# Performance work log

Hardware: AMD Instinct MI355X
Metric: run time of the kernel (lower is better)

The kernel has to match this reference:

```python
import jax, jax.numpy as jnp
import numpy as np
import math

B, T, D_MODEL, N_HEADS = 4, 2048, 1024, 16
HEAD_DIM = D_MODEL // N_HEADS


def setup_inputs() -> dict:
    key = jax.random.key(0)
    k1, k2, k3 = jax.random.split(key, 3)
    x = jax.random.normal(k1, (B, T, D_MODEL), dtype=jnp.float32)
    # torch Linear weight layout: [out_features, in_features]
    w_qkv = jax.random.normal(k2, (3 * D_MODEL, D_MODEL), dtype=jnp.float32) * (1.0 / math.sqrt(D_MODEL))
    w_out = jax.random.normal(k3, (D_MODEL, D_MODEL), dtype=jnp.float32) * (1.0 / math.sqrt(D_MODEL))
    return {"x": x, "w_qkv": w_qkv, "w_out": w_out}


def reference(x, w_qkv, w_out):
    b, t, c = x.shape
    h, d = N_HEADS, HEAD_DIM
    # qkv projection: (B,T,3C) -> (3,B,H,T,D)
    qkv = jnp.einsum('btc,fc->btf', x, w_qkv)
    qkv = qkv.reshape(b, t, 3, h, d).transpose(2, 0, 3, 1, 4)
    q, k, v = qkv[0], qkv[1], qkv[2]
    scale = 1.0 / math.sqrt(d)
    # full O(T^2) attention scores, causal masked
    scores = jnp.einsum('bhqd,bhkd->bhqk', q, k) * scale
    causal = jnp.tril(jnp.ones((t, t), dtype=bool))
    scores = jnp.where(causal[None, None, :, :], scores, jnp.float32(-jnp.inf))
    attn = jax.nn.softmax(scores, axis=-1)
    out = jnp.einsum('bhqk,bhkd->bhqd', attn, v)  # (B,H,T,D)
    out = out.transpose(0, 2, 1, 3).reshape(b, t, c)
    out = jnp.einsum('btc,oc->bto', out, w_out)
    return out
```

## Files before the change

kernel.cpp:

```cpp
#include <hip/hip_runtime.h>
#include <hip/hip_bf16.h>

#define T_SEQ 2048
#define BATCH 4
#define NH    16
#define DM    1024
#define HD    64

typedef __attribute__((ext_vector_type(4))) float  f32x4;
typedef __attribute__((ext_vector_type(8))) short  s16x8;
typedef __attribute__((ext_vector_type(4))) short  s16x4;
typedef __attribute__((ext_vector_type(4))) unsigned short u16x4;

__device__ __forceinline__ unsigned short f2b(float f) {
  union { float f; unsigned u; } v; v.f = f;
  unsigned u = v.u;
  unsigned r = 0x7fffu + ((u >> 16) & 1u);
  u += r;
  return (unsigned short)(u >> 16);
}

__device__ __forceinline__ f32x4 mfma16(s16x8 a, s16x8 b, f32x4 c) {
  return __builtin_amdgcn_mfma_f32_16x16x32_bf16(a, b, c, 0, 0, 0);
}

__global__ void cvt_f32_bf16(const float* __restrict__ src,
                             unsigned short* __restrict__ dst, int n4) {
  int i = blockIdx.x * blockDim.x + threadIdx.x;
  int stride = gridDim.x * blockDim.x;
  for (int j = i; j < n4; j += stride) {
    f32x4 v = ((const f32x4*)src)[j];
    s16x4 o;
    o.x = (short)f2b(v.x); o.y = (short)f2b(v.y);
    o.z = (short)f2b(v.z); o.w = (short)f2b(v.w);
    ((s16x4*)dst)[j] = o;
  }
}

template<int OUT_F32>
__global__ __launch_bounds__(256)
void gemm_bt(const unsigned short* __restrict__ A,
             const unsigned short* __restrict__ B,
             void* __restrict__ C, int M, int N, int K) {
  __shared__ unsigned short As[128 * 32];
  __shared__ unsigned short Bs[128 * 32];
  const int tid  = threadIdx.x;
  const int lane = tid & 63;
  const int w    = tid >> 6;
  const int wr   = w >> 1, wc = w & 1;
  const int lr   = lane & 15, g = lane >> 4;

  const int gx  = gridDim.x, nwg = gx * gridDim.y;
  const int bid = blockIdx.y * gx + blockIdx.x;
  const int qq  = nwg >> 3;
  const int b2  = (bid & 7) * qq + (bid >> 3);
  const int row0 = (b2 % gx) * 128;
  const int col0 = (b2 / gx) * 128;

  const int srow = w * 16 + (lane >> 2);
  const int scol = (lane & 3) * 8;

  f32x4 acc[4][4] = {};

  for (int kt = 0; kt < K; kt += 32) {
    __syncthreads();
#pragma unroll
    for (int s = 0; s < 2; ++s) {
      const unsigned short* srcA = A + (size_t)(row0 + s * 64 + srow) * K + kt + scol;
      __builtin_amdgcn_global_load_lds((const void*)srcA, (void*)&As[(s * 64 + w * 16) * 32], 16, 0, 0);
      const unsigned short* srcB = B + (size_t)(col0 + s * 64 + srow) * K + kt + scol;
      __builtin_amdgcn_global_load_lds((const void*)srcB, (void*)&Bs[(s * 64 + w * 16) * 32], 16, 0, 0);
    }
    __syncthreads();

    s16x8 af[4], bf[4];
#pragma unroll
    for (int m = 0; m < 4; ++m)
      af[m] = *(const s16x8*)&As[(wr * 64 + m * 16 + lr) * 32 + g * 8];
#pragma unroll
    for (int n = 0; n < 4; ++n)
      bf[n] = *(const s16x8*)&Bs[(wc * 64 + n * 16 + lr) * 32 + g * 8];
#pragma unroll
    for (int m = 0; m < 4; ++m)
#pragma unroll
      for (int n = 0; n < 4; ++n)
        acc[m][n] = mfma16(af[m], bf[n], acc[m][n]);
  }

#pragma unroll
  for (int m = 0; m < 4; ++m)
#pragma unroll
    for (int n = 0; n < 4; ++n)
#pragma unroll
      for (int i = 0; i < 4; ++i) {
        int row = row0 + wr * 64 + m * 16 + g * 4 + i;
        int col = col0 + wc * 64 + n * 16 + lr;
        if (OUT_F32)
          ((float*)C)[(size_t)row * N + col] = acc[m][n][i];
        else
          ((unsigned short*)C)[(size_t)row * N + col] = f2b(acc[m][n][i]);
      }
}

__global__ __launch_bounds__(512)
void attn_kernel(const unsigned short* __restrict__ qkv,
                 unsigned short* __restrict__ out) {
  __shared__ unsigned short Ks[2][64 * 64];
  __shared__ unsigned short Vt[2][64 * 72];
  __shared__ unsigned short Ps[8][16 * 72];

  const int tid  = threadIdx.x;
  const int lane = tid & 63;
  const int w    = tid >> 6;
  const int lr   = lane & 15, g = lane >> 4;
  const int bh   = blockIdx.x;
  const int qt   = 15 - (int)blockIdx.y;
  const int b    = bh >> 4, h = bh & 15;
  const int q0   = qt * 128;
  const int qr   = q0 + w * 16;
  const int qq   = qr + lr;
  const size_t rb = (size_t)b * T_SEQ;

  s16x8 qf[2];
  {
    const unsigned short* qp = qkv + (rb + qq) * 3072 + h * 64;
    qf[0] = *(const s16x8*)(qp + g * 8);
    qf[1] = *(const s16x8*)(qp + 32 + g * 8);
  }

  float mI = -1e30f, lI = 0.f;
  f32x4 o[4] = {};

  const int nt   = 2 * qt + 2;
  const int qmax = qr + 15;

  const bool grpV = (tid < 256);
  const int vd0 = (tid & 7) * 8, vr0 = (tid >> 3) * 2;
  const int t2  = tid - 256;
  const int kr0 = t2 >> 3, kc0 = t2 & 7;

  s16x8 pre0, pre1;
  {
    if (grpV) {
      const unsigned short* vp = &qkv[(rb + vr0) * 3072 + 2048 + h * 64 + vd0];
      pre0 = *(const s16x8*)vp;
      pre1 = *(const s16x8*)(vp + 3072);
    } else {
      const unsigned short* kp = &qkv[(rb + kr0) * 3072 + 1024 + h * 64 + kc0 * 8];
      pre0 = *(const s16x8*)kp;
      pre1 = *(const s16x8*)(kp + 32 * 3072);
    }
  }

  for (int t = 0; t < nt; ++t) {
    const int cur = t & 1;
    if (grpV) {
#pragma unroll
      for (int jj = 0; jj < 8; ++jj) {
        int d = vd0 + jj;
        int sw = ((d ^ (d >> 3)) & 7) << 4;
        unsigned val = (unsigned)(unsigned short)pre0[jj] |
                       ((unsigned)(unsigned short)pre1[jj] << 16);
        *(unsigned*)((char*)&Vt[cur][0] + d * 144 + ((vr0 * 2) ^ sw)) = val;
      }
    } else {
      *(s16x8*)((char*)&Ks[cur][0] + kr0 * 128 + ((kc0 * 16) ^ ((kr0 & 7) << 4))) = pre0;
      int kr1 = kr0 + 32;
      *(s16x8*)((char*)&Ks[cur][0] + kr1 * 128 + ((kc0 * 16) ^ ((kr1 & 7) << 4))) = pre1;
    }
    if (t + 1 < nt) {
      const int kv0n = (t + 1) * 64;
      if (grpV) {
        const unsigned short* vp = &qkv[(rb + kv0n + vr0) * 3072 + 2048 + h * 64 + vd0];
        pre0 = *(const s16x8*)vp;
        pre1 = *(const s16x8*)(vp + 3072);
      } else {
        const unsigned short* kp = &qkv[(rb + kv0n + kr0) * 3072 + 1024 + h * 64 + kc0 * 8];
        pre0 = *(const s16x8*)kp;
        pre1 = *(const s16x8*)(kp + 32 * 3072);
      }
    }
    __syncthreads();

    const int kv0 = t * 64;
    if (kv0 <= qmax) {
      f32x4 s4[4];
      __builtin_amdgcn_s_setprio(1);
#pragma unroll
      for (int kc = 0; kc < 4; ++kc) {
        int row = kc * 16 + lr;
        const char* kbase = (const char*)&Ks[cur][0] + row * 128;
        int sw = (row & 7) << 4;
        s16x8 kf0 = *(const s16x8*)(kbase + ((g * 16) ^ sw));
        s16x8 kf1 = *(const s16x8*)(kbase + ((64 + g * 16) ^ sw));
        f32x4 s = {};
        s = mfma16(kf0, qf[0], s);
        s = mfma16(kf1, qf[1], s);
        s4[kc] = s;
      }
      __builtin_amdgcn_s_setprio(0);

#pragma unroll
      for (int kc = 0; kc < 4; ++kc)
#pragma unroll
        for (int i = 0; i < 4; ++i) {
          int key = kv0 + kc * 16 + g * 4 + i;
          float v = s4[kc][i] * 0.125f;
          s4[kc][i] = (key <= qq) ? v : -1e30f;
        }

      float mx0 = fmaxf(fmaxf(s4[0][0], s4[0][1]), fmaxf(s4[0][2], s4[0][3]));
      float mx1 = fmaxf(fmaxf(s4[1][0], s4[1][1]), fmaxf(s4[1][2], s4[1][3]));
      float mx2 = fmaxf(fmaxf(s4[2][0], s4[2][1]), fmaxf(s4[2][2], s4[2][3]));
      float mx3 = fmaxf(fmaxf(s4[3][0], s4[3][1]), fmaxf(s4[3][2], s4[3][3]));
      float mx = fmaxf(fmaxf(mx0, mx1), fmaxf(mx2, mx3));
      mx = fmaxf(mx, __shfl_xor(mx, 16));
      mx = fmaxf(mx, __shfl_xor(mx, 32));
      float mn = fmaxf(mI, mx);
      float alpha = __expf(mI - mn);
      mI = mn;
      float rs = 0.f;
#pragma unroll
      for (int kc = 0; kc < 4; ++kc)
#pragma unroll
        for (int i = 0; i < 4; ++i) {
          float p = __expf(s4[kc][i] - mn);
          s4[kc][i] = p;
          rs += p;
        }
      rs += __shfl_xor(rs, 16);
      rs += __shfl_xor(rs, 32);
      lI = lI * alpha + rs;

      {
        char* pw = (char*)&Ps[w][0] + lr * 144;
#pragma unroll
        for (int kc = 0; kc < 4; ++kc) {
          unsigned v0 = (unsigned)f2b(s4[kc][0]) | ((unsigned)f2b(s4[kc][1]) << 16);
          unsigned v1 = (unsigned)f2b(s4[kc][2]) | ((unsigned)f2b(s4[kc][3]) << 16);
          *(unsigned*)(pw + kc * 32 + g * 8)     = v0;
          *(unsigned*)(pw + kc * 32 + g * 8 + 4) = v1;
        }
      }

#pragma unroll
      for (int n = 0; n < 4; ++n)
#pragma unroll
        for (int i = 0; i < 4; ++i)
          o[n][i] *= alpha;

      asm volatile("s_waitcnt lgkmcnt(0)" ::: "memory");

      __builtin_amdgcn_s_setprio(1);
#pragma unroll
      for (int kk = 0; kk < 2; ++kk) {
        s16x8 pf = *(const s16x8*)((const char*)&Ps[w][0] + lr * 144 + kk * 64 + g * 16);
#pragma unroll
        for (int n = 0; n < 4; ++n) {
          int d = n * 16 + lr;
          int sw = ((d ^ (d >> 3)) & 7) << 4;
          s16x8 vf = *(const s16x8*)((const char*)&Vt[cur][0] + d * 144 + ((kk * 64 + g * 16) ^ sw));
          o[n] = mfma16(vf, pf, o[n]);
        }
      }
      __builtin_amdgcn_s_setprio(0);
    }
  }

  float rl = 1.f / lI;
#pragma unroll
  for (int n = 0; n < 4; ++n) {
    u16x4 pk;
#pragma unroll
    for (int i = 0; i < 4; ++i) pk[i] = f2b(o[n][i] * rl);
    *(u16x4*)&out[(rb + qq) * 1024 + h * 64 + n * 16 + g * 4] = pk;
  }
}

extern "C" void kernel_launch(void* const* d_in, const int* in_sizes, int n_in,
                              void* d_out, int out_size, void* d_ws, size_t ws_size,
                              hipStream_t stream) {
  const float* x     = (const float*)d_in[0];
  const float* w_qkv = (const float*)d_in[1];
  const float* w_out = (const float*)d_in[2];

  const size_t n_x   = (size_t)BATCH * T_SEQ * DM;
  const size_t n_wq  = (size_t)3 * DM * DM;
  const size_t n_wo  = (size_t)DM * DM;
  const size_t n_qkv = (size_t)BATCH * T_SEQ * 3 * DM;
  const size_t need  = (n_x + n_wq + n_wo + n_qkv + n_x) * 2;
  if (ws_size < need) return;

  unsigned short* xb  = (unsigned short*)d_ws;
  unsigned short* wqb = xb + n_x;
  unsigned short* wob = wqb + n_wq;
  unsigned short* qkv = wob + n_wo;
  unsigned short* att = qkv + n_qkv;

  cvt_f32_bf16<<<2048, 256, 0, stream>>>(x, xb, (int)(n_x / 4));
  cvt_f32_bf16<<<1024, 256, 0, stream>>>(w_qkv, wqb, (int)(n_wq / 4));
  cvt_f32_bf16<<<512, 256, 0, stream>>>(w_out, wob, (int)(n_wo / 4));

  gemm_bt<0><<<dim3(64, 24), 256, 0, stream>>>(xb, wqb, qkv, BATCH * T_SEQ, 3 * DM, DM);
  attn_kernel<<<dim3(BATCH * NH, T_SEQ / 128), 512, 0, stream>>>(qkv, att);
  gemm_bt<1><<<dim3(64, 8), 256, 0, stream>>>(att, wob, d_out, BATCH * T_SEQ, DM, DM);
}
```

Before: 212.3 us.

## Fold softmax scale into Q weights, mask only diagonal tiles, defer rescaling

The three f32-to-bf16 conversion launches are merged into a single kernel. That kernel also scales the Q rows of w_qkv by 1/8, which removes the per-score multiply in attention. Causal masking now runs only on tiles that cross the diagonal. The online softmax skips the max update and the output rescale when the new block max exceeds the running max by at most 8 across the wave, in the style of FA4 lazy rescaling. This trades exp-range headroom for fewer VALU ops. Folding the scale into the weights before bf16 rounding slightly changes numerics.

```diff
diff --git a/kernel.cpp b/kernel.cpp
--- a/kernel.cpp
+++ b/kernel.cpp
@@ -24,16 +24,28 @@
   return __builtin_amdgcn_mfma_f32_16x16x32_bf16(a, b, c, 0, 0, 0);
 }
 
-__global__ void cvt_f32_bf16(const float* __restrict__ src,
-                             unsigned short* __restrict__ dst, int n4) {
+__global__ void cvt_all(const float* __restrict__ x, const float* __restrict__ wq,
+                        const float* __restrict__ wo,
+                        unsigned short* __restrict__ xb, unsigned short* __restrict__ wqb,
+                        unsigned short* __restrict__ wob) {
+  const int N4X = (BATCH * T_SEQ * DM) / 4;
+  const int N4Q = (3 * DM * DM) / 4;
+  const int N4O = (DM * DM) / 4;
+  const int N4QSCALED = (DM * DM) / 4;
   int i = blockIdx.x * blockDim.x + threadIdx.x;
   int stride = gridDim.x * blockDim.x;
-  for (int j = i; j < n4; j += stride) {
-    f32x4 v = ((const f32x4*)src)[j];
+  for (int j = i; j < N4X + N4Q + N4O; j += stride) {
+    const float* src; unsigned short* dst; int k; float scale = 1.f;
+    if (j < N4X) { src = x; dst = xb; k = j; }
+    else if (j < N4X + N4Q) {
+      k = j - N4X; src = wq; dst = wqb;
+      if (k < N4QSCALED) scale = 0.125f;
+    } else { k = j - N4X - N4Q; src = wo; dst = wob; }
+    f32x4 v = ((const f32x4*)src)[k];
     s16x4 o;
-    o.x = (short)f2b(v.x); o.y = (short)f2b(v.y);
-    o.z = (short)f2b(v.z); o.w = (short)f2b(v.w);
-    ((s16x4*)dst)[j] = o;
+    o.x = (short)f2b(v.x * scale); o.y = (short)f2b(v.y * scale);
+    o.z = (short)f2b(v.z * scale); o.w = (short)f2b(v.w * scale);
+    ((s16x4*)dst)[k] = o;
   }
 }
 
@@ -200,31 +212,38 @@
       }
       __builtin_amdgcn_s_setprio(0);
 
-#pragma unroll
-      for (int kc = 0; kc < 4; ++kc)
-#pragma unroll
-        for (int i = 0; i < 4; ++i) {
-          int key = kv0 + kc * 16 + g * 4 + i;
-          float v = s4[kc][i] * 0.125f;
-          s4[kc][i] = (key <= qq) ? v : -1e30f;
-        }
-
-      float mx0 = fmaxf(fmaxf(s4[0][0], s4[0][1]), fmaxf(s4[0][2], s4[0][3]));
-      float mx1 = fmaxf(fmaxf(s4[1][0], s4[1][1]), fmaxf(s4[1][2], s4[1][3]));
-      float mx2 = fmaxf(fmaxf(s4[2][0], s4[2][1]), fmaxf(s4[2][2], s4[2][3]));
-      float mx3 = fmaxf(fmaxf(s4[3][0], s4[3][1]), fmaxf(s4[3][2], s4[3][3]));
-      float mx = fmaxf(fmaxf(mx0, mx1), fmaxf(mx2, mx3));
+      if (kv0 + 63 > qr) {
+#pragma unroll
+        for (int kc = 0; kc < 4; ++kc)
+#pragma unroll
+          for (int i = 0; i < 4; ++i) {
+            int key = kv0 + kc * 16 + g * 4 + i;
+            if (key > qq) s4[kc][i] = -1e30f;
+          }
+      }
+
+      float mx = fmaxf(fmaxf(fmaxf(s4[0][0], s4[0][1]), fmaxf(s4[0][2], s4[0][3])),
+                 fmaxf(fmaxf(fmaxf(s4[1][0], s4[1][1]), fmaxf(s4[1][2], s4[1][3])),
+                 fmaxf(fmaxf(fmaxf(s4[2][0], s4[2][1]), fmaxf(s4[2][2], s4[2][3])),
+                       fmaxf(fmaxf(s4[3][0], s4[3][1]), fmaxf(s4[3][2], s4[3][3])))));
       mx = fmaxf(mx, __shfl_xor(mx, 16));
       mx = fmaxf(mx, __shfl_xor(mx, 32));
-      float mn = fmaxf(mI, mx);
-      float alpha = __expf(mI - mn);
-      mI = mn;
+
+      const bool defer = __all(mx - mI <= 8.f);
+      float alpha;
+      if (defer) {
+        alpha = 1.f;
+      } else {
+        float mn = fmaxf(mI, mx);
+        alpha = __expf(mI - mn);
+        mI = mn;
+      }
       float rs = 0.f;
 #pragma unroll
       for (int kc = 0; kc < 4; ++kc)
 #pragma unroll
         for (int i = 0; i < 4; ++i) {
-          float p = __expf(s4[kc][i] - mn);
+          float p = __expf(s4[kc][i] - mI);
           s4[kc][i] = p;
           rs += p;
         }
@@ -243,11 +262,13 @@
         }
       }
 
-#pragma unroll
-      for (int n = 0; n < 4; ++n)
-#pragma unroll
-        for (int i = 0; i < 4; ++i)
-          o[n][i] *= alpha;
+      if (!defer) {
+#pragma unroll
+        for (int n = 0; n < 4; ++n)
+#pragma unroll
+          for (int i = 0; i < 4; ++i)
+            o[n][i] *= alpha;
+      }
 
       asm volatile("s_waitcnt lgkmcnt(0)" ::: "memory");
 
@@ -297,9 +318,7 @@
   unsigned short* qkv = wob + n_wo;
   unsigned short* att = qkv + n_qkv;
 
-  cvt_f32_bf16<<<2048, 256, 0, stream>>>(x, xb, (int)(n_x / 4));
-  cvt_f32_bf16<<<1024, 256, 0, stream>>>(w_qkv, wqb, (int)(n_wq / 4));
-  cvt_f32_bf16<<<512, 256, 0, stream>>>(w_out, wob, (int)(n_wo / 4));
+  cvt_all<<<2048, 256, 0, stream>>>(x, w_qkv, w_out, xb, wqb, wob);
 
   gemm_bt<0><<<dim3(64, 24), 256, 0, stream>>>(xb, wqb, qkv, BATCH * T_SEQ, 3 * DM, DM);
   attn_kernel<<<dim3(BATCH * NH, T_SEQ / 128), 512, 0, stream>>>(qkv, att);
```

New measurement: 204.6 us. 1.04x faster.
